# Optimization experiments

Measured on AMD Instinct MI355X. Metric: run time of the kernel, lower is better.

The kernel has to match this reference:

```python
import jax, jax.numpy as jnp
import numpy as np

DIM = 768
HEADS = 12
HEAD_DIM = DIM // HEADS          # 64
M = int(DIM * 0.5)               # 384 random features
HIDDEN = int(DIM * 4.0)          # 3072
SCALE = HEAD_DIM ** (-0.25)
EPSILON = 1e-8
LN_EPS = 1e-5


def _orf(key):
    # per-head block-orthogonal random features, scaled by sqrt(m)
    def one(k):
        a = jax.random.normal(k, (M, HEAD_DIM))
        q, _ = jnp.linalg.qr(a)          # (M, HEAD_DIM), orthonormal columns
        return q.T                        # (HEAD_DIM, M), orthonormal rows
    ks = jax.random.split(key, HEADS)
    return jax.vmap(one)(ks) * np.sqrt(M)  # (H, HEAD_DIM, M)


def setup_inputs() -> dict:
    key = jax.random.key(0)
    ks = jax.random.split(key, 8)
    s = 0.02
    return {
        "x": jax.random.normal(ks[0], (32, 1024, DIM), jnp.float32),
        "ln1_g": jnp.ones((DIM,), jnp.float32),
        "ln1_b": jnp.zeros((DIM,), jnp.float32),
        "qkv_w": jax.random.normal(ks[1], (DIM, 3 * DIM), jnp.float32) * s,
        "qkv_b": jnp.zeros((3 * DIM,), jnp.float32),
        "w_orf": _orf(ks[2]).astype(jnp.float32),
        "proj_w": jax.random.normal(ks[3], (DIM, DIM), jnp.float32) * s,
        "proj_b": jnp.zeros((DIM,), jnp.float32),
        "ln2_g": jnp.ones((DIM,), jnp.float32),
        "ln2_b": jnp.zeros((DIM,), jnp.float32),
        "fc1_w": jax.random.normal(ks[4], (DIM, HIDDEN), jnp.float32) * s,
        "fc1_b": jnp.zeros((HIDDEN,), jnp.float32),
        "fc2_w": jax.random.normal(ks[5], (HIDDEN, DIM), jnp.float32) * s,
        "fc2_b": jnp.zeros((DIM,), jnp.float32),
    }


def _layernorm(x, g, b):
    mu = jnp.mean(x, axis=-1, keepdims=True)
    var = jnp.mean(jnp.square(x - mu), axis=-1, keepdims=True)
    return (x - mu) * jax.lax.rsqrt(var + LN_EPS) * g + b


def _feature_map(x, w):
    # x: (B,H,N,C), w: (H,C,M) -> exp(x*scale @ w - ||x*scale||^2/2)/sqrt(M)
    xs = x * SCALE
    proj = jnp.einsum("bhnc,hcm->bhnm", xs, w)
    sq = 0.5 * jnp.sum(xs * xs, axis=-1, keepdims=True)
    return jnp.exp(proj - sq) / np.sqrt(M)


def _performer_attn(x, qkv_w, qkv_b, w_orf, proj_w, proj_b):
    B, N, _ = x.shape
    qkv = x @ qkv_w + qkv_b                       # (B,N,3*DIM)
    qkv = qkv.reshape(B, N, 3, HEADS, HEAD_DIM)
    qkv = jnp.transpose(qkv, (2, 0, 3, 1, 4))     # (3,B,H,N,C)
    q = _feature_map(qkv[0], w_orf)               # (B,H,N,M)
    k = _feature_map(qkv[1], w_orf)               # (B,H,N,M)
    v = qkv[2]                                    # (B,H,N,C)
    k_sum = jnp.sum(k, axis=2)                    # (B,H,M)
    D = jnp.einsum("bhnm,bhm->bhn", q, k_sum)[..., None] + EPSILON
    ktv = jnp.einsum("bhnm,bhnc->bhmc", k, v)     # (B,H,M,C)
    out = jnp.einsum("bhnm,bhmc->bhnc", q, ktv) / D
    out = jnp.transpose(out, (0, 2, 1, 3)).reshape(B, N, DIM)
    return out @ proj_w + proj_b


def reference(x, ln1_g, ln1_b, qkv_w, qkv_b, w_orf, proj_w, proj_b,
              ln2_g, ln2_b, fc1_w, fc1_b, fc2_w, fc2_b):
    h = x + _performer_attn(_layernorm(x, ln1_g, ln1_b),
                            qkv_w, qkv_b, w_orf, proj_w, proj_b)
    y = _layernorm(h, ln2_g, ln2_b)
    y = jax.nn.gelu(y @ fc1_w + fc1_b) @ fc2_w + fc2_b
    return h + y
```

## Files before the change

kernel.cpp:

```cpp
#include <hip/hip_runtime.h>
#include <hip/hip_bf16.h>

#define NTOK   32768
#define BATCH  32
#define SEQ    1024
#define DIMD   768
#define HEADS  12
#define HDIM   64
#define MFEAT  384
#define HIDDEN 3072
#define SCALE  0.35355339059327379f
#define HALF_SCALE2 0.0625f
#define EPSP   3.84e-6f
#define WSCL   64.0f
#define SCA_ONE   0x7F7F7F7Fu
#define SCB_I64   0x79797979u

typedef __attribute__((ext_vector_type(8))) short bf16x8;
typedef __attribute__((ext_vector_type(4))) float f32x4;
typedef __attribute__((ext_vector_type(2))) long long llong2;
typedef __attribute__((ext_vector_type(8))) int i32x8;

static __device__ __forceinline__ float bf2f(unsigned short u) {
    return __uint_as_float(((unsigned)u) << 16);
}
static __device__ __forceinline__ unsigned short f2bf(float f) {
    unsigned u = __float_as_uint(f);
    return (unsigned short)((u + 0x7FFFu + ((u >> 16) & 1u)) >> 16);
}
static __device__ __forceinline__ unsigned char f2e4m3(float f) {
    unsigned u = __float_as_uint(f);
    const unsigned char s = (unsigned char)((u >> 24) & 0x80);
    const float af = __uint_as_float(u & 0x7FFFFFFF);
    if (!(af < 464.0f)) return s | 0x7E;
    int e = (int)((u >> 23) & 0xFF) - 127;
    if (e < -6) e = -6;
    const float ulp = __uint_as_float((unsigned)((e - 3 + 127) << 23));
    const float q = rintf(af / ulp) * ulp;
    if (q == 0.0f) return s;
    const unsigned v = __float_as_uint(q);
    const int qe = (int)((v >> 23) & 0xFF) - 127;
    if (qe < -6) return s | (unsigned char)(q * 512.0f);
    return s | (unsigned char)(((qe + 7) << 3) | ((v >> 20) & 7));
}
static __device__ __forceinline__ unsigned char f2e4m3_hw(float v) {
    unsigned r = 0;
    asm("v_cvt_pk_fp8_f32 %0, %1, %1" : "+v"(r) : "v"(v));
    return (unsigned char)(r & 0xFF);
}
static __device__ __forceinline__ int kp128(int kl) {
    return (((kl >> 4) & 1) << 6) + ((kl >> 5) << 4) + (kl & 15);
}
static __device__ __forceinline__ float gelu_fast(float v) {
    const float c = 0.7978845608028654f;
    const float u = c * v * (1.0f + 0.044715f * v * v);
    return v * __builtin_amdgcn_rcpf(1.0f + __expf(-2.0f * u));
}
static __device__ __forceinline__ void gload16(const void* g, void* l) {
    __builtin_amdgcn_global_load_lds(
        (const __attribute__((address_space(1))) void*)g,
        (__attribute__((address_space(3))) void*)l, 16, 0, 0);
}

template <int OT>
__global__ __launch_bounds__(256) void ln_vec(
    const float* __restrict__ x, const float* __restrict__ g,
    const float* __restrict__ bta, void* __restrict__ o) {
    const size_t row = blockIdx.x;
    const float* xr = x + row * DIMD;
    const int t = threadIdx.x;
    float4 v = make_float4(0.f, 0.f, 0.f, 0.f);
    if (t < 192) v = *(const float4*)(xr + t * 4);
    float s  = v.x + v.y + v.z + v.w;
    float sq = v.x * v.x + v.y * v.y + v.z * v.z + v.w * v.w;
    const int lane = t & 63, w = t >> 6;
    #pragma unroll
    for (int off = 32; off > 0; off >>= 1) {
        s  += __shfl_down(s, off, 64);
        sq += __shfl_down(sq, off, 64);
    }
    __shared__ float red[2][4];
    if (lane == 0) { red[0][w] = s; red[1][w] = sq; }
    __syncthreads();
    s  = red[0][0] + red[0][1] + red[0][2] + red[0][3];
    sq = red[1][0] + red[1][1] + red[1][2] + red[1][3];
    const float mu  = s * (1.0f / DIMD);
    const float var = sq * (1.0f / DIMD) - mu * mu;
    const float r = rsqrtf(var + 1e-5f);
    if (t < 192) {
        const float4 gv = *(const float4*)(g + t * 4);
        const float4 bv = *(const float4*)(bta + t * 4);
        const float o0 = (v.x - mu) * r * gv.x + bv.x;
        const float o1 = (v.y - mu) * r * gv.y + bv.y;
        const float o2 = (v.z - mu) * r * gv.z + bv.z;
        const float o3 = (v.w - mu) * r * gv.w + bv.w;
        if constexpr (OT == 1) {
            unsigned short* orow = (unsigned short*)o + row * DIMD + t * 4;
            *(ushort4*)orow = make_ushort4(f2bf(o0), f2bf(o1), f2bf(o2), f2bf(o3));
        } else {
            const int k = t * 4;
            const int gb = k & ~127, kl = k & 127;
            unsigned char* orow = (unsigned char*)o + row * DIMD + gb + kp128(kl);
            uchar4 p; p.x = f2e4m3(o0); p.y = f2e4m3(o1);
            p.z = f2e4m3(o2); p.w = f2e4m3(o3);
            *(uchar4*)orow = p;
        }
    }
}

__global__ __launch_bounds__(256) void wconv(
    const float* __restrict__ W, unsigned short* __restrict__ Wt, int K, int N) {
    __shared__ float tile[32][33];
    const int n0 = blockIdx.x << 5, k0 = blockIdx.y << 5;
    const int tn = threadIdx.x & 31, tg = threadIdx.x >> 5;
    #pragma unroll
    for (int i = 0; i < 4; ++i) {
        const int k = (tg << 2) + i;
        tile[k][tn] = W[(size_t)(k0 + k) * N + n0 + tn];
    }
    __syncthreads();
    #pragma unroll
    for (int i = 0; i < 4; ++i) {
        const int n = (tg << 2) + i;
        Wt[(size_t)(n0 + n) * K + k0 + tn] = f2bf(tile[tn][n]);
    }
}

__global__ __launch_bounds__(256) void wconv_f8(
    const float* __restrict__ W, unsigned char* __restrict__ Wt, int K, int N) {
    __shared__ float tile[32][33];
    const int n0 = blockIdx.x << 5, k0 = blockIdx.y << 5;
    const int tn = threadIdx.x & 31, tg = threadIdx.x >> 5;
    #pragma unroll
    for (int i = 0; i < 4; ++i) {
        const int k = (tg << 2) + i;
        tile[k][tn] = W[(size_t)(k0 + k) * N + n0 + tn];
    }
    __syncthreads();
    #pragma unroll
    for (int i = 0; i < 4; ++i) {
        const int n = (tg << 2) + i;
        const int k = k0 + tn;
        const int gb = k & ~127, kl = k & 127;
        Wt[(size_t)(n0 + n) * K + gb + kp128(kl)] = f2e4m3(WSCL * tile[tn][n]);
    }
}

__global__ __launch_bounds__(256) void wprep(
    const float* __restrict__ worf, unsigned short* __restrict__ worf_ts) {
    __shared__ float tile[32][33];
    const int m0 = blockIdx.x << 5, c0 = blockIdx.y << 5, h = blockIdx.z;
    const int tn = threadIdx.x & 31, tg = threadIdx.x >> 5;
    #pragma unroll
    for (int i = 0; i < 4; ++i) {
        const int c = (tg << 2) + i;
        tile[c][tn] = worf[(size_t)(h * HDIM + c0 + c) * MFEAT + m0 + tn];
    }
    __syncthreads();
    #pragma unroll
    for (int i = 0; i < 4; ++i) {
        const int m = (tg << 2) + i;
        worf_ts[(size_t)(h * MFEAT + m0 + m) * HDIM + c0 + tn] =
            f2bf(SCALE * tile[tn][m]);
    }
}

template <int ACT, bool RES, bool OBF16>
__global__ __launch_bounds__(256, 2) void gemm_mfma(
    const unsigned short* __restrict__ A, const unsigned short* __restrict__ Wt,
    const float* __restrict__ bias, const float* __restrict__ resid,
    void* __restrict__ Craw, int K, int N) {
    __shared__ unsigned short As0[2][4096], As1[2][4096];
    __shared__ unsigned short Bs0[2][4096], Bs1[2][4096];
    const int t = threadIdx.x;
    const int w = t >> 6, l = t & 63;
    const int ncol = gridDim.x;
    const int lin = blockIdx.y * ncol + blockIdx.x;
    const int cpx = (ncol * gridDim.y) >> 3;
    const int wg = (lin & 7) * cpx + (lin >> 3);
    const int row0 = (wg / ncol) << 7, col0 = (wg % ncol) << 7;
    const int wr = (w >> 1) << 6, wc = (w & 1) << 6;

    const int sc = (((l & 3) ^ ((l >> 3) & 3)) << 3);
    const size_t arow0 = (size_t)(row0 + w * 32 + (l >> 2)) * K;
    const size_t arow1 = arow0 + (size_t)16 * K;
    const size_t brow0 = (size_t)(col0 + w * 32 + (l >> 2)) * K;
    const size_t brow1 = brow0 + (size_t)16 * K;

    f32x4 acc[4][4] = {};
    const int NT = K >> 6;

    auto stage = [&](int bi, int s) {
        const size_t ko = (size_t)s << 6;
        gload16(A + arow0 + ko + sc,      &As0[bi][w * 1024]);
        gload16(A + arow1 + ko + sc,      &As0[bi][w * 1024 + 512]);
        gload16(A + arow0 + ko + 32 + sc, &As1[bi][w * 1024]);
        gload16(A + arow1 + ko + 32 + sc, &As1[bi][w * 1024 + 512]);
        gload16(Wt + brow0 + ko + sc,      &Bs0[bi][w * 1024]);
        gload16(Wt + brow1 + ko + sc,      &Bs0[bi][w * 1024 + 512]);
        gload16(Wt + brow0 + ko + 32 + sc, &Bs1[bi][w * 1024]);
        gload16(Wt + brow1 + ko + 32 + sc, &Bs1[bi][w * 1024 + 512]);
    };

    stage(0, 0);
    const int lr = l & 15, lg = l >> 4;
    const int xoff = ((lg ^ ((lr >> 1) & 3)) << 3);
    for (int s = 0; s < NT; ++s) {
        asm volatile("s_waitcnt vmcnt(0)" ::: "memory");
        __builtin_amdgcn_s_barrier();
        __builtin_amdgcn_sched_barrier(0);
        if (s + 1 < NT) stage((s + 1) & 1, s + 1);
        const unsigned short* a0 = &As0[s & 1][0];
        const unsigned short* a1 = &As1[s & 1][0];
        const unsigned short* b0 = &Bs0[s & 1][0];
        const unsigned short* b1 = &Bs1[s & 1][0];
        bf16x8 af[4][2], bfr[4][2];
        #pragma unroll
        for (int f = 0; f < 4; ++f) {
            const int ra = ((wr + f * 16 + lr) << 5) + xoff;
            const int rb = ((wc + f * 16 + lr) << 5) + xoff;
            af[f][0]  = *(const bf16x8*)(a0 + ra);
            af[f][1]  = *(const bf16x8*)(a1 + ra);
            bfr[f][0] = *(const bf16x8*)(b0 + rb);
            bfr[f][1] = *(const bf16x8*)(b1 + rb);
        }
        #pragma unroll
        for (int ks = 0; ks < 2; ++ks)
            #pragma unroll
            for (int fi = 0; fi < 4; ++fi)
                #pragma unroll
                for (int fj = 0; fj < 4; ++fj)
                    acc[fi][fj] = __builtin_amdgcn_mfma_f32_16x16x32_bf16(
                        af[fi][ks], bfr[fj][ks], acc[fi][fj], 0, 0, 0);
    }

    float bv[4];
    #pragma unroll
    for (int fj = 0; fj < 4; ++fj) bv[fj] = bias[col0 + wc + fj * 16 + lr];
    #pragma unroll
    for (int fi = 0; fi < 4; ++fi) {
        #pragma unroll
        for (int r = 0; r < 4; ++r) {
            const int row = row0 + wr + fi * 16 + lg * 4 + r;
            const size_t base = (size_t)row * N + col0 + wc + lr;
            #pragma unroll
            for (int fj = 0; fj < 4; ++fj) {
                float v = acc[fi][fj][r] + bv[fj];
                if constexpr (RES) v += resid[base + fj * 16];
                if constexpr (ACT == 1) v = gelu_fast(v);
                if constexpr (OBF16) ((unsigned short*)Craw)[base + fj * 16] = f2bf(v);
                else                 ((float*)Craw)[base + fj * 16] = v;
            }
        }
    }
}

template <int ACT, bool RES, int OT>
__global__ __launch_bounds__(256, 2) void gemm_mx(
    const unsigned char* __restrict__ A, const unsigned char* __restrict__ Wt,
    const float* __restrict__ bias, const float* __restrict__ resid,
    void* __restrict__ Craw, int K, int N) {
    __shared__ unsigned char As0[2][8192], As1[2][8192];
    __shared__ unsigned char Bs0[2][8192], Bs1[2][8192];
    const int t = threadIdx.x;
    const int w = t >> 6, l = t & 63;
    const int ncol = gridDim.x;
    const int lin = blockIdx.y * ncol + blockIdx.x;
    const int cpx = (ncol * gridDim.y) >> 3;
    const int wg = (lin & 7) * cpx + (lin >> 3);
    const int row0 = (wg / ncol) << 7, col0 = (wg % ncol) << 7;
    const int wr = (w >> 1) << 6, wc = (w & 1) << 6;

    const int sc = (((l & 3) ^ ((l >> 3) & 3)) << 4);
    const size_t arow0 = (size_t)(row0 + w * 32 + (l >> 2)) * K;
    const size_t arow1 = arow0 + (size_t)16 * K;
    const size_t brow0 = (size_t)(col0 + w * 32 + (l >> 2)) * K;
    const size_t brow1 = brow0 + (size_t)16 * K;

    f32x4 acc[4][4] = {};
    const int NT = K >> 7;

    auto stage = [&](int bi, int s) {
        const size_t ko = (size_t)s << 7;
        gload16(A + arow0 + ko + sc,      &As0[bi][w * 2048]);
        gload16(A + arow1 + ko + sc,      &As0[bi][w * 2048 + 1024]);
        gload16(A + arow0 + ko + 64 + sc, &As1[bi][w * 2048]);
        gload16(A + arow1 + ko + 64 + sc, &As1[bi][w * 2048 + 1024]);
        gload16(Wt + brow0 + ko + sc,      &Bs0[bi][w * 2048]);
        gload16(Wt + brow1 + ko + sc,      &Bs0[bi][w * 2048 + 1024]);
        gload16(Wt + brow0 + ko + 64 + sc, &Bs1[bi][w * 2048]);
        gload16(Wt + brow1 + ko + 64 + sc, &Bs1[bi][w * 2048 + 1024]);
    };

    stage(0, 0);
    const int lr = l & 15, lg = l >> 4;
    const int xoff = ((lg ^ ((lr >> 1) & 3)) << 4);
    for (int s = 0; s < NT; ++s) {
        asm volatile("s_waitcnt vmcnt(0)" ::: "memory");
        __builtin_amdgcn_s_barrier();
        __builtin_amdgcn_sched_barrier(0);
        if (s + 1 < NT) stage((s + 1) & 1, s + 1);
        const unsigned char* a0 = &As0[s & 1][0];
        const unsigned char* a1 = &As1[s & 1][0];
        const unsigned char* b0 = &Bs0[s & 1][0];
        const unsigned char* b1 = &Bs1[s & 1][0];
        i32x8 afm[4], bfm[4];
        #pragma unroll
        for (int f = 0; f < 4; ++f) {
            const int ra = ((wr + f * 16 + lr) << 6) + xoff;
            const int rb = ((wc + f * 16 + lr) << 6) + xoff;
            ((llong2*)&afm[f])[0] = *(const llong2*)(a0 + ra);
            ((llong2*)&afm[f])[1] = *(const llong2*)(a1 + ra);
            ((llong2*)&bfm[f])[0] = *(const llong2*)(b0 + rb);
            ((llong2*)&bfm[f])[1] = *(const llong2*)(b1 + rb);
        }
        #pragma unroll
        for (int fi = 0; fi < 4; ++fi)
            #pragma unroll
            for (int fj = 0; fj < 4; ++fj)
                acc[fi][fj] = __builtin_amdgcn_mfma_scale_f32_16x16x128_f8f6f4(
                    afm[fi], bfm[fj], acc[fi][fj], 0, 0,
                    0, SCA_ONE, 0, SCB_I64);
    }

    float bv[4];
    #pragma unroll
    for (int fj = 0; fj < 4; ++fj) bv[fj] = bias[col0 + wc + fj * 16 + lr];
    #pragma unroll
    for (int fi = 0; fi < 4; ++fi) {
        #pragma unroll
        for (int r = 0; r < 4; ++r) {
            const int row = row0 + wr + fi * 16 + lg * 4 + r;
            const size_t base = (size_t)row * N + col0 + wc + lr;
            #pragma unroll
            for (int fj = 0; fj < 4; ++fj) {
                float v = acc[fi][fj][r] + bv[fj];
                if constexpr (RES) v += resid[base + fj * 16];
                if constexpr (ACT == 1) v = gelu_fast(v);
                if constexpr (OT == 2) {
                    const int cl = wc + fj * 16 + lr;
                    ((unsigned char*)Craw)[(size_t)row * N + col0 + kp128(cl)] =
                        f2e4m3_hw(v);
                } else {
                    ((float*)Craw)[base + fj * 16] = v;
                }
            }
        }
    }
}

__global__ __launch_bounds__(256, 1) void ktv_mfma(
    const unsigned short* __restrict__ qkvb,
    const unsigned short* __restrict__ worf_ts,
    unsigned short* __restrict__ ktvT) {
    const int h = blockIdx.x, b = blockIdx.y, bh = b * HEADS + h;
    __shared__ __align__(16) unsigned short Klds[32][72];
    __shared__ __align__(16) unsigned short VT[80][40];
    __shared__ __align__(16) unsigned short P[4][96][40];
    const int t = threadIdx.x, w = t >> 6, l = t & 63;
    const int lr = l & 15, lg = l >> 4;
    const int m0 = w * 96;

    bf16x8 bfw[6][2];
    #pragma unroll
    for (int mt = 0; mt < 6; ++mt)
        #pragma unroll
        for (int ks = 0; ks < 2; ++ks)
            bfw[mt][ks] = *(const bf16x8*)(worf_ts +
                (size_t)(h * MFEAT + m0 + mt * 16 + lr) * HDIM + ks * 32 + lg * 8);

    f32x4 acc[5][6] = {};

    for (int i = t; i < 16 * 40; i += 256) {
        const int r = 64 + i / 40, cc = i % 40;
        VT[r][cc] = (r == 64) ? (unsigned short)0x3F80 : (unsigned short)0;
    }
    const unsigned short* kglob = qkvb + (size_t)b * SEQ * 2304 + 768 + h * 64;
    const unsigned short* vglob = kglob + 768;

    for (int n0 = 0; n0 < SEQ; n0 += 32) {
        __syncthreads();
        {
            const int row = t >> 3, c8 = (t & 7) << 3;
            *(bf16x8*)&Klds[row][c8] =
                *(const bf16x8*)(kglob + (size_t)(n0 + row) * 2304 + c8);
        }
        {
            const int n = t & 31, c0 = (t >> 5) << 3;
            const unsigned short* src = vglob + (size_t)(n0 + n) * 2304 + c0;
            ushort4 v0 = *(const ushort4*)src;
            ushort4 v1 = *(const ushort4*)(src + 4);
            VT[c0 + 0][n] = v0.x; VT[c0 + 1][n] = v0.y;
            VT[c0 + 2][n] = v0.z; VT[c0 + 3][n] = v0.w;
            VT[c0 + 4][n] = v1.x; VT[c0 + 5][n] = v1.y;
            VT[c0 + 6][n] = v1.z; VT[c0 + 7][n] = v1.w;
        }
        __syncthreads();

        bf16x8 afk[2][2];
        float sqv[2][4];
        #pragma unroll
        for (int ns = 0; ns < 2; ++ns) {
            float s = 0.f;
            #pragma unroll
            for (int ks = 0; ks < 2; ++ks) {
                afk[ns][ks] = *(const bf16x8*)&Klds[ns * 16 + lr][ks * 32 + lg * 8];
                #pragma unroll
                for (int j = 0; j < 8; ++j) {
                    const float f = bf2f((unsigned short)afk[ns][ks][j]);
                    s += f * f;
                }
            }
            s += __shfl_xor(s, 16);
            s += __shfl_xor(s, 32);
            s *= HALF_SCALE2;
            #pragma unroll
            for (int r = 0; r < 4; ++r)
                sqv[ns][r] = __shfl(s, (lg << 2) + r);
        }

        #pragma unroll
        for (int mt = 0; mt < 6; ++mt) {
            #pragma unroll
            for (int ns = 0; ns < 2; ++ns) {
                f32x4 p = {};
                p = __builtin_amdgcn_mfma_f32_16x16x32_bf16(afk[ns][0], bfw[mt][0], p, 0, 0, 0);
                p = __builtin_amdgcn_mfma_f32_16x16x32_bf16(afk[ns][1], bfw[mt][1], p, 0, 0, 0);
                ushort4 pk;
                pk.x = f2bf(__expf(p[0] - sqv[ns][0]));
                pk.y = f2bf(__expf(p[1] - sqv[ns][1]));
                pk.z = f2bf(__expf(p[2] - sqv[ns][2]));
                pk.w = f2bf(__expf(p[3] - sqv[ns][3]));
                *(ushort4*)&P[w][mt * 16 + lr][ns * 16 + lg * 4] = pk;
            }
        }
        asm volatile("s_waitcnt lgkmcnt(0)" ::: "memory");
        __builtin_amdgcn_sched_barrier(0);

        bf16x8 afv[5];
        #pragma unroll
        for (int ct = 0; ct < 5; ++ct)
            afv[ct] = *(const bf16x8*)&VT[ct * 16 + lr][lg * 8];
        #pragma unroll
        for (int mt = 0; mt < 6; ++mt) {
            const bf16x8 bp = *(const bf16x8*)&P[w][mt * 16 + lr][lg * 8];
            #pragma unroll
            for (int ct = 0; ct < 5; ++ct)
                acc[ct][mt] = __builtin_amdgcn_mfma_f32_16x16x32_bf16(afv[ct], bp, acc[ct][mt], 0, 0, 0);
        }
    }

    unsigned short* dst = ktvT + (size_t)bh * 80 * MFEAT;
    #pragma unroll
    for (int ct = 0; ct < 5; ++ct)
        #pragma unroll
        for (int mt = 0; mt < 6; ++mt)
            #pragma unroll
            for (int r = 0; r < 4; ++r) {
                const int cc = ct * 16 + lg * 4 + r;
                const int m = m0 + mt * 16 + lr;
                dst[(size_t)cc * MFEAT + m] = f2bf(acc[ct][mt][r]);
            }
}

__global__ __launch_bounds__(256) void attn_out_mfma(
    const unsigned short* __restrict__ qkvb,
    const unsigned short* __restrict__ worf_ts,
    const unsigned short* __restrict__ ktvT,
    unsigned short* __restrict__ attn) {
    const int n0 = blockIdx.x << 7;
    const int h = blockIdx.y, b = blockIdx.z, bh = b * HEADS + h;
    __shared__ __align__(16) unsigned short KT[80][104];
    __shared__ __align__(16) unsigned short P[4][32][104];
    const int t = threadIdx.x, w = t >> 6, l = t & 63;
    const int lr = l & 15, lg = l >> 4;
    const int nw = n0 + w * 32;

    bf16x8 bq[2][2];
    float sqn[2];
    #pragma unroll
    for (int nt = 0; nt < 2; ++nt) {
        float s = 0.f;
        #pragma unroll
        for (int ks = 0; ks < 2; ++ks) {
            bq[nt][ks] = *(const bf16x8*)(qkvb +
                (size_t)(b * SEQ + nw + nt * 16 + lr) * 2304 + h * 64 + ks * 32 + lg * 8);
            #pragma unroll
            for (int j = 0; j < 8; ++j) {
                const float f = bf2f((unsigned short)bq[nt][ks][j]);
                s += f * f;
            }
        }
        s += __shfl_xor(s, 16);
        s += __shfl_xor(s, 32);
        sqn[nt] = s * HALF_SCALE2;
    }

    f32x4 acc[5][2] = {};
    const unsigned short* ktg = ktvT + (size_t)bh * 80 * MFEAT;

    for (int ch = 0; ch < 4; ++ch) {
        const int m0 = ch * 96;
        __syncthreads();
        for (int i = t; i < 1920; i += 256) {
            const int row = i / 24, q = i % 24;
            *(ushort4*)&KT[row][q * 4] =
                *(const ushort4*)(ktg + (size_t)row * MFEAT + m0 + q * 4);
        }
        __syncthreads();

        #pragma unroll
        for (int mt = 0; mt < 6; ++mt) {
            bf16x8 afw[2];
            #pragma unroll
            for (int ks = 0; ks < 2; ++ks)
                afw[ks] = *(const bf16x8*)(worf_ts +
                    (size_t)(h * MFEAT + m0 + mt * 16 + lr) * HDIM + ks * 32 + lg * 8);
            #pragma unroll
            for (int nt = 0; nt < 2; ++nt) {
                f32x4 p = {};
                p = __builtin_amdgcn_mfma_f32_16x16x32_bf16(afw[0], bq[nt][0], p, 0, 0, 0);
                p = __builtin_amdgcn_mfma_f32_16x16x32_bf16(afw[1], bq[nt][1], p, 0, 0, 0);
                ushort4 pk;
                pk.x = f2bf(__expf(p[0] - sqn[nt]));
                pk.y = f2bf(__expf(p[1] - sqn[nt]));
                pk.z = f2bf(__expf(p[2] - sqn[nt]));
                pk.w = f2bf(__expf(p[3] - sqn[nt]));
                *(ushort4*)&P[w][nt * 16 + lr][mt * 16 + lg * 4] = pk;
            }
        }
        asm volatile("s_waitcnt lgkmcnt(0)" ::: "memory");
        __builtin_amdgcn_sched_barrier(0);

        #pragma unroll
        for (int ks = 0; ks < 3; ++ks) {
            bf16x8 bp[2];
            #pragma unroll
            for (int nt = 0; nt < 2; ++nt)
                bp[nt] = *(const bf16x8*)&P[w][nt * 16 + lr][ks * 32 + lg * 8];
            #pragma unroll
            for (int ct = 0; ct < 5; ++ct) {
                const bf16x8 av = *(const bf16x8*)&KT[ct * 16 + lr][ks * 32 + lg * 8];
                #pragma unroll
                for (int nt = 0; nt < 2; ++nt)
                    acc[ct][nt] = __builtin_amdgcn_mfma_f32_16x16x32_bf16(av, bp[nt], acc[ct][nt], 0, 0, 0);
            }
        }
    }

    #pragma unroll
    for (int nt = 0; nt < 2; ++nt) {
        const float d = __shfl(acc[4][nt][0], lr);
        const float inv = 1.0f / (d + EPSP);
        const int token = b * SEQ + nw + nt * 16 + lr;
        #pragma unroll
        for (int ct = 0; ct < 4; ++ct)
            #pragma unroll
            for (int r = 0; r < 4; ++r) {
                const int cc = ct * 16 + lg * 4 + r;
                attn[(size_t)token * DIMD + h * 64 + cc] = f2bf(acc[ct][nt][r] * inv);
            }
    }
}

extern "C" void kernel_launch(void* const* d_in, const int* in_sizes, int n_in,
                              void* d_out, int out_size, void* d_ws, size_t ws_size,
                              hipStream_t stream) {
    const float* x      = (const float*)d_in[0];
    const float* ln1_g  = (const float*)d_in[1];
    const float* ln1_b  = (const float*)d_in[2];
    const float* qkv_w  = (const float*)d_in[3];
    const float* qkv_b  = (const float*)d_in[4];
    const float* w_orf  = (const float*)d_in[5];
    const float* proj_w = (const float*)d_in[6];
    const float* proj_b = (const float*)d_in[7];
    const float* ln2_g  = (const float*)d_in[8];
    const float* ln2_b  = (const float*)d_in[9];
    const float* fc1_w  = (const float*)d_in[10];
    const float* fc1_b  = (const float*)d_in[11];
    const float* fc2_w  = (const float*)d_in[12];
    const float* fc2_b  = (const float*)d_in[13];
    float* out = (float*)d_out;

    char* wsb = (char*)d_ws;
    unsigned short* qkvb    = (unsigned short*)wsb;
    unsigned short* attn    = (unsigned short*)(wsb + 150994944);
    unsigned short* ktvT    = (unsigned short*)(wsb + 201326592);
    unsigned short* worf_ts = (unsigned short*)(wsb + 224919552);
    unsigned char*  y2f8    = (unsigned char*)(wsb + 201326592);
    unsigned char*  hidf8   = (unsigned char*)wsb;
    unsigned short* qkv_wt  = (unsigned short*)(wsb + 251658240);
    unsigned short* proj_wt = (unsigned short*)(wsb + 255197184);
    unsigned char*  fc1_wf8 = (unsigned char*)(wsb + 256376832);
    unsigned char*  fc2_wf8 = (unsigned char*)(wsb + 261095424);
    unsigned short* xln     = (unsigned short*)d_out;

    wconv<<<dim3(2304 / 32, 768 / 32), 256, 0, stream>>>(qkv_w, qkv_wt, DIMD, 2304);
    wconv<<<dim3(768 / 32, 768 / 32), 256, 0, stream>>>(proj_w, proj_wt, DIMD, DIMD);
    wconv_f8<<<dim3(3072 / 32, 768 / 32), 256, 0, stream>>>(fc1_w, fc1_wf8, DIMD, HIDDEN);
    wconv_f8<<<dim3(768 / 32, 3072 / 32), 256, 0, stream>>>(fc2_w, fc2_wf8, HIDDEN, DIMD);
    wprep<<<dim3(MFEAT / 32, HDIM / 32, HEADS), 256, 0, stream>>>(w_orf, worf_ts);
    ln_vec<1><<<NTOK, 256, 0, stream>>>(x, ln1_g, ln1_b, xln);
    gemm_mfma<0, false, true><<<dim3(2304 / 128, NTOK / 128), 256, 0, stream>>>(
        xln, qkv_wt, qkv_b, nullptr, qkvb, DIMD, 2304);
    ktv_mfma<<<dim3(HEADS, BATCH), 256, 0, stream>>>(qkvb, worf_ts, ktvT);
    attn_out_mfma<<<dim3(SEQ / 128, HEADS, BATCH), 256, 0, stream>>>(
        qkvb, worf_ts, ktvT, attn);
    gemm_mfma<0, true, false><<<dim3(DIMD / 128, NTOK / 128), 256, 0, stream>>>(
        attn, proj_wt, proj_b, x, out, DIMD, DIMD);
    ln_vec<2><<<NTOK, 256, 0, stream>>>(out, ln2_g, ln2_b, y2f8);
    gemm_mx<1, false, 2><<<dim3(HIDDEN / 128, NTOK / 128), 256, 0, stream>>>(
        y2f8, fc1_wf8, fc1_b, nullptr, hidf8, DIMD, HIDDEN);
    gemm_mx<0, true, 0><<<dim3(DIMD / 128, NTOK / 128), 256, 0, stream>>>(
        hidf8, fc2_wf8, fc2_b, out, out, HIDDEN, DIMD);
}
```

Baseline: 756.1 us.

## Add triple-buffered BK32 GEMM for projection and pack bf16 stores

Adds a second GEMM variant with a K-tile of 32 and three shared-memory stages, so two tiles are prefetched ahead, and uses it for the attention output projection. The existing BK64 GEMM is kept for QKV. Separately, the feature-map and attention-output bf16 conversions now use paired hardware conversion intrinsics with 64-bit packed stores instead of per-element rounding and scalar stores. The aim is to cut load latency stalls in the projection GEMM and reduce ALU and store instruction counts, at the cost of more barriers per K step.

```diff
diff --git a/kernel.cpp b/kernel.cpp
--- a/kernel.cpp
+++ b/kernel.cpp
@@ -27,6 +27,14 @@
 static __device__ __forceinline__ unsigned short f2bf(float f) {
     unsigned u = __float_as_uint(f);
     return (unsigned short)((u + 0x7FFFu + ((u >> 16) & 1u)) >> 16);
+}
+static __device__ __forceinline__ uint2 pk4bf(float e0, float e1, float e2, float e3) {
+    const __hip_bfloat162 lo = __float22bfloat162_rn(make_float2(e0, e1));
+    const __hip_bfloat162 hi = __float22bfloat162_rn(make_float2(e2, e3));
+    uint2 r;
+    r.x = *(const unsigned*)&lo;
+    r.y = *(const unsigned*)&hi;
+    return r;
 }
 static __device__ __forceinline__ unsigned char f2e4m3(float f) {
     unsigned u = __float_as_uint(f);
@@ -166,7 +174,7 @@
 }
 
 template <int ACT, bool RES, bool OBF16>
-__global__ __launch_bounds__(256, 2) void gemm_mfma(
+__global__ __launch_bounds__(256, 2) void gemm_bk64(
     const unsigned short* __restrict__ A, const unsigned short* __restrict__ Wt,
     const float* __restrict__ bias, const float* __restrict__ resid,
     void* __restrict__ Craw, int K, int N) {
@@ -232,6 +240,91 @@
                 for (int fj = 0; fj < 4; ++fj)
                     acc[fi][fj] = __builtin_amdgcn_mfma_f32_16x16x32_bf16(
                         af[fi][ks], bfr[fj][ks], acc[fi][fj], 0, 0, 0);
+    }
+
+    float bv[4];
+    #pragma unroll
+    for (int fj = 0; fj < 4; ++fj) bv[fj] = bias[col0 + wc + fj * 16 + lr];
+    #pragma unroll
+    for (int fi = 0; fi < 4; ++fi) {
+        #pragma unroll
+        for (int r = 0; r < 4; ++r) {
+            const int row = row0 + wr + fi * 16 + lg * 4 + r;
+            const size_t base = (size_t)row * N + col0 + wc + lr;
+            #pragma unroll
+            for (int fj = 0; fj < 4; ++fj) {
+                float v = acc[fi][fj][r] + bv[fj];
+                if constexpr (RES) v += resid[base + fj * 16];
+                if constexpr (ACT == 1) v = gelu_fast(v);
+                if constexpr (OBF16) ((unsigned short*)Craw)[base + fj * 16] = f2bf(v);
+                else                 ((float*)Craw)[base + fj * 16] = v;
+            }
+        }
+    }
+}
+
+template <int ACT, bool RES, bool OBF16>
+__global__ __launch_bounds__(256, 2) void gemm_bk32(
+    const unsigned short* __restrict__ A, const unsigned short* __restrict__ Wt,
+    const float* __restrict__ bias, const float* __restrict__ resid,
+    void* __restrict__ Craw, int K, int N) {
+    __shared__ unsigned short As[3][128 * 32];
+    __shared__ unsigned short Bs[3][128 * 32];
+    const int t = threadIdx.x;
+    const int w = t >> 6, l = t & 63;
+    const int ncol = gridDim.x;
+    const int lin = blockIdx.y * ncol + blockIdx.x;
+    const int cpx = (ncol * gridDim.y) >> 3;
+    const int wg = (lin & 7) * cpx + (lin >> 3);
+    const int row0 = (wg / ncol) << 7, col0 = (wg % ncol) << 7;
+    const int wr = (w >> 1) << 6, wc = (w & 1) << 6;
+
+    const int sc = (((l & 3) ^ ((l >> 3) & 3)) << 3);
+    const unsigned short* ag0 = A  + (size_t)(row0 + w * 32 + (l >> 2)) * K + sc;
+    const unsigned short* ag1 = ag0 + (size_t)16 * K;
+    const unsigned short* bg0 = Wt + (size_t)(col0 + w * 32 + (l >> 2)) * K + sc;
+    const unsigned short* bg1 = bg0 + (size_t)16 * K;
+
+    f32x4 acc[4][4] = {};
+    const int NT = K >> 5;
+
+    auto stage = [&](int bi, int s) {
+        const size_t ko = (size_t)s << 5;
+        gload16(ag0 + ko, &As[bi][w * 1024]);
+        gload16(ag1 + ko, &As[bi][w * 1024 + 512]);
+        gload16(bg0 + ko, &Bs[bi][w * 1024]);
+        gload16(bg1 + ko, &Bs[bi][w * 1024 + 512]);
+    };
+
+    stage(0, 0);
+    stage(1, 1);
+    const int lr = l & 15, lg = l >> 4;
+    const int lkx = (lg << 3) ^ ((((lr >> 1) & 3)) << 3);
+    int cur = 0;
+    for (int s = 0; s < NT; ++s) {
+        if (s + 1 < NT) asm volatile("s_waitcnt vmcnt(4)" ::: "memory");
+        else            asm volatile("s_waitcnt vmcnt(0)" ::: "memory");
+        __builtin_amdgcn_s_barrier();
+        __builtin_amdgcn_sched_barrier(0);
+        if (s + 2 < NT) {
+            int sb = cur + 2; if (sb >= 3) sb -= 3;
+            stage(sb, s + 2);
+        }
+        const unsigned short* ab = &As[cur][0];
+        const unsigned short* bb = &Bs[cur][0];
+        bf16x8 af[4], bfr[4];
+        #pragma unroll
+        for (int f = 0; f < 4; ++f) {
+            af[f]  = *(const bf16x8*)(ab + (wr + f * 16 + lr) * 32 + lkx);
+            bfr[f] = *(const bf16x8*)(bb + (wc + f * 16 + lr) * 32 + lkx);
+        }
+        #pragma unroll
+        for (int fi = 0; fi < 4; ++fi)
+            #pragma unroll
+            for (int fj = 0; fj < 4; ++fj)
+                acc[fi][fj] = __builtin_amdgcn_mfma_f32_16x16x32_bf16(
+                    af[fi], bfr[fj], acc[fi][fj], 0, 0, 0);
+        cur = (cur + 1 == 3) ? 0 : cur + 1;
     }
 
     float bv[4];
@@ -426,12 +519,9 @@
                 f32x4 p = {};
                 p = __builtin_amdgcn_mfma_f32_16x16x32_bf16(afk[ns][0], bfw[mt][0], p, 0, 0, 0);
                 p = __builtin_amdgcn_mfma_f32_16x16x32_bf16(afk[ns][1], bfw[mt][1], p, 0, 0, 0);
-                ushort4 pk;
-                pk.x = f2bf(__expf(p[0] - sqv[ns][0]));
-                pk.y = f2bf(__expf(p[1] - sqv[ns][1]));
-                pk.z = f2bf(__expf(p[2] - sqv[ns][2]));
-                pk.w = f2bf(__expf(p[3] - sqv[ns][3]));
-                *(ushort4*)&P[w][mt * 16 + lr][ns * 16 + lg * 4] = pk;
+                const uint2 pk2 = pk4bf(__expf(p[0] - sqv[ns][0]), __expf(p[1] - sqv[ns][1]),
+                                        __expf(p[2] - sqv[ns][2]), __expf(p[3] - sqv[ns][3]));
+                *(uint2*)&P[w][mt * 16 + lr][ns * 16 + lg * 4] = pk2;
             }
         }
         asm volatile("s_waitcnt lgkmcnt(0)" ::: "memory");
@@ -521,12 +611,9 @@
                 f32x4 p = {};
                 p = __builtin_amdgcn_mfma_f32_16x16x32_bf16(afw[0], bq[nt][0], p, 0, 0, 0);
                 p = __builtin_amdgcn_mfma_f32_16x16x32_bf16(afw[1], bq[nt][1], p, 0, 0, 0);
-                ushort4 pk;
-                pk.x = f2bf(__expf(p[0] - sqn[nt]));
-                pk.y = f2bf(__expf(p[1] - sqn[nt]));
-                pk.z = f2bf(__expf(p[2] - sqn[nt]));
-                pk.w = f2bf(__expf(p[3] - sqn[nt]));
-                *(ushort4*)&P[w][nt * 16 + lr][mt * 16 + lg * 4] = pk;
+                const uint2 pk2 = pk4bf(__expf(p[0] - sqn[nt]), __expf(p[1] - sqn[nt]),
+                                        __expf(p[2] - sqn[nt]), __expf(p[3] - sqn[nt]));
+                *(uint2*)&P[w][nt * 16 + lr][mt * 16 + lg * 4] = pk2;
             }
         }
         asm volatile("s_waitcnt lgkmcnt(0)" ::: "memory");
@@ -554,12 +641,11 @@
         const float inv = 1.0f / (d + EPSP);
         const int token = b * SEQ + nw + nt * 16 + lr;
         #pragma unroll
-        for (int ct = 0; ct < 4; ++ct)
-            #pragma unroll
-            for (int r = 0; r < 4; ++r) {
-                const int cc = ct * 16 + lg * 4 + r;
-                attn[(size_t)token * DIMD + h * 64 + cc] = f2bf(acc[ct][nt][r] * inv);
-            }
+        for (int ct = 0; ct < 4; ++ct) {
+            const uint2 o2 = pk4bf(acc[ct][nt][0] * inv, acc[ct][nt][1] * inv,
+                                   acc[ct][nt][2] * inv, acc[ct][nt][3] * inv);
+            *(uint2*)&attn[(size_t)token * DIMD + h * 64 + ct * 16 + lg * 4] = o2;
+        }
     }
 }
 
@@ -601,12 +687,12 @@
     wconv_f8<<<dim3(768 / 32, 3072 / 32), 256, 0, stream>>>(fc2_w, fc2_wf8, HIDDEN, DIMD);
     wprep<<<dim3(MFEAT / 32, HDIM / 32, HEADS), 256, 0, stream>>>(w_orf, worf_ts);
     ln_vec<1><<<NTOK, 256, 0, stream>>>(x, ln1_g, ln1_b, xln);
-    gemm_mfma<0, false, true><<<dim3(2304 / 128, NTOK / 128), 256, 0, stream>>>(
+    gemm_bk64<0, false, true><<<dim3(2304 / 128, NTOK / 128), 256, 0, stream>>>(
         xln, qkv_wt, qkv_b, nullptr, qkvb, DIMD, 2304);
     ktv_mfma<<<dim3(HEADS, BATCH), 256, 0, stream>>>(qkvb, worf_ts, ktvT);
     attn_out_mfma<<<dim3(SEQ / 128, HEADS, BATCH), 256, 0, stream>>>(
         qkvb, worf_ts, ktvT, attn);
-    gemm_mfma<0, true, false><<<dim3(DIMD / 128, NTOK / 128), 256, 0, stream>>>(
+    gemm_bk32<0, true, false><<<dim3(DIMD / 128, NTOK / 128), 256, 0, stream>>>(
         attn, proj_wt, proj_b, x, out, DIMD, DIMD);
     ln_vec<2><<<NTOK, 256, 0, stream>>>(out, ln2_g, ln2_b, y2f8);
     gemm_mx<1, false, 2><<<dim3(HIDDEN / 128, NTOK / 128), 256, 0, stream>>>(
```

Result: faster. 740.3 us (median of 2 runs) (-2.1%).
